# Kernel optimization log

Hardware: AMD Instinct MI355X
Metric: run time of the kernel (lower is better)

Reference implementation:

```python
import jax, jax.numpy as jnp
import numpy as np

B, L, C = 2, 2048, 1024
H = 16
D = C // H  # 64
ROPE_THETA = 10000.0


def _rope_tables(seq_len, head_dim, dtype=jnp.float32):
    # freqs_cis equivalent: angle[t, j] = t * theta^(-2j/head_dim)
    inv_freq = 1.0 / (ROPE_THETA ** (jnp.arange(0, head_dim, 2, dtype=jnp.float32) / head_dim))
    ang = jnp.arange(seq_len, dtype=jnp.float32)[:, None] * inv_freq[None, :]  # [L, D/2]
    return jnp.cos(ang).astype(dtype), jnp.sin(ang).astype(dtype)


def setup_inputs() -> dict:
    key = jax.random.key(0)
    k1, k2, k3 = jax.random.split(key, 3)
    x = jax.random.normal(k1, (B, L, C), dtype=jnp.float32)
    qkv_w = jax.random.normal(k2, (3 * C, C), dtype=jnp.float32) * 0.02
    proj_w = jax.random.normal(k3, (C, C), dtype=jnp.float32) * 0.02
    proj_b = jnp.zeros((C,), dtype=jnp.float32)
    cos, sin = _rope_tables(L, D)
    return {"x": x, "qkv_w": qkv_w, "proj_w": proj_w, "proj_b": proj_b, "cos": cos, "sin": sin}


def _apply_rope(t, cos, sin):
    # t: [B, L, H, D]; cos/sin: [L, D/2]; interleaved complex rotation
    te = t[..., 0::2]
    to = t[..., 1::2]
    c = cos[None, :, None, :]
    s = sin[None, :, None, :]
    re = te * c - to * s
    im = te * s + to * c
    out = jnp.stack([re, im], axis=-1)  # [B, L, H, D/2, 2]
    return out.reshape(t.shape)


def reference(x, qkv_w, proj_w, proj_b, cos, sin):
    b, l, c = x.shape
    scale = (c // H) ** -0.5
    qkv = (x @ qkv_w.T).reshape(b, l, 3, H, c // H)  # [B, L, 3, H, D]
    q, k, v = qkv[:, :, 0], qkv[:, :, 1], qkv[:, :, 2]  # each [B, L, H, D]
    q = _apply_rope(q, cos, sin)
    k = _apply_rope(k, cos, sin)
    # memory_efficient_attention math: softmax(q k^T * scale) v, per head
    logits = jnp.einsum("blhd,bmhd->bhlm", q, k) * scale  # [B, H, L, L]
    p = jax.nn.softmax(logits, axis=-1)
    out = jnp.einsum("bhlm,bmhd->blhd", p, v).reshape(b, l, c)
    return out @ proj_w.T + proj_b
```

## Files before the change

kernel.cpp:

```cpp
#include <hip/hip_runtime.h>


typedef __attribute__((ext_vector_type(8))) short s8v;
typedef __attribute__((ext_vector_type(4))) float f4v;
typedef __attribute__((ext_vector_type(4))) unsigned short u16x4;

__device__ __forceinline__ unsigned short f2bf(float f) {
  unsigned int u = __float_as_uint(f);
  u += 0x7FFFu + ((u >> 16) & 1u);
  return (unsigned short)(u >> 16);
}

__device__ __forceinline__ void gl16(const unsigned short* g, unsigned short* l) {
  __builtin_amdgcn_global_load_lds((const __attribute__((address_space(1))) void*)g,
                                   (__attribute__((address_space(3))) void*)l,
                                   16, 0, 0);
}

__device__ __forceinline__ s8v pack8(const float* p) {
  const float4 a = *reinterpret_cast<const float4*>(p);
  const float4 b = *reinterpret_cast<const float4*>(p + 4);
  s8v r;
  r[0]=(short)f2bf(a.x); r[1]=(short)f2bf(a.y); r[2]=(short)f2bf(a.z); r[3]=(short)f2bf(a.w);
  r[4]=(short)f2bf(b.x); r[5]=(short)f2bf(b.y); r[6]=(short)f2bf(b.z); r[7]=(short)f2bf(b.w);
  return r;
}

#define DPP_F(x, ctrl) \
  __int_as_float(__builtin_amdgcn_update_dpp(0, __float_as_int(x), (ctrl), 0xf, 0xf, false))

__device__ __forceinline__ float row16_max(float x) {
  x = fmaxf(x, DPP_F(x, 0xB1));
  x = fmaxf(x, DPP_F(x, 0x4E));
  x = fmaxf(x, DPP_F(x, 0x124));
  x = fmaxf(x, DPP_F(x, 0x128));
  return x;
}
__device__ __forceinline__ float row16_sum(float x) {
  x += DPP_F(x, 0xB1);
  x += DPP_F(x, 0x4E);
  x += DPP_F(x, 0x124);
  x += DPP_F(x, 0x128);
  return x;
}

__global__ __launch_bounds__(256)
void k_convert(const float* __restrict__ X, const float* __restrict__ W,
               const float* __restrict__ Wp,
               unsigned short* __restrict__ Xb, unsigned short* __restrict__ Wb,
               unsigned short* __restrict__ Wpb)
{
  const int bid = blockIdx.x, tid = threadIdx.x;
  if (bid < 2048) {
    const size_t e = (size_t)bid * 2048 + (size_t)tid * 8;
    *reinterpret_cast<s8v*>(Xb + e) = pack8(X + e);
  } else if (bid < 3584) {
    const size_t e = (size_t)(bid - 2048) * 2048 + (size_t)tid * 8;
    const int p = (int)(e >> 10);
    const int col = (int)(e & 1023);
    int n;
    if (p < 2048) {
      const int t = p >> 10;
      const int hh = (p & 1023) >> 6;
      const int c = p & 63;
      const int d = (c < 32) ? (c << 1) : (((c - 32) << 1) | 1);
      n = (t << 10) + (hh << 6) + d;
    } else {
      n = p;
    }
    *reinterpret_cast<s8v*>(Wb + e) = pack8(W + (size_t)n * 1024 + col);
  } else {
    const size_t e = (size_t)(bid - 3584) * 2048 + (size_t)tid * 8;
    *reinterpret_cast<s8v*>(Wpb + e) = pack8(Wp + e);
  }
}

__global__ __launch_bounds__(256)
void k_gemm_qkv(const unsigned short* __restrict__ Ab,
                const unsigned short* __restrict__ Bb,
                const float* __restrict__ Ct, const float* __restrict__ St,
                unsigned short* __restrict__ qb, unsigned short* __restrict__ kb,
                unsigned short* __restrict__ vt)
{
  __shared__ __align__(16) unsigned short Asm[128 * 32];
  __shared__ __align__(16) unsigned short Bsm[128 * 32];

  const int tid  = threadIdx.x;
  const int w    = tid >> 6;
  const int lane = tid & 63;
  const int lr   = lane & 15;
  const int lg   = lane >> 4;
  const int wm   = w >> 1, wn = w & 1;

  const int row0 = blockIdx.x << 7;
  const int col0 = blockIdx.y << 7;

  const int srow = (w << 5) + (lane >> 2);
  const int scol = (lane & 3) << 3;
  const unsigned short* Ag = Ab + (size_t)(row0 + srow) * 1024 + scol;
  const unsigned short* Bg = Bb + (size_t)(col0 + srow) * 1024 + scol;
  unsigned short* Al0 = &Asm[(w << 5) * 32];
  unsigned short* Al1 = Al0 + 512;
  unsigned short* Bl0 = &Bsm[(w << 5) * 32];
  unsigned short* Bl1 = Bl0 + 512;

  f4v acc[4][4];
#pragma unroll
  for (int m = 0; m < 4; ++m)
#pragma unroll
    for (int n = 0; n < 4; ++n) acc[m][n] = (f4v){0.f, 0.f, 0.f, 0.f};

  for (int k0 = 0; k0 < 1024; k0 += 32) {
    gl16(Ag + k0, Al0);
    gl16(Ag + k0 + 16 * 1024, Al1);
    gl16(Bg + k0, Bl0);
    gl16(Bg + k0 + 16 * 1024, Bl1);
    __syncthreads();

    s8v af[4], bfr[4];
#pragma unroll
    for (int m = 0; m < 4; ++m)
      af[m] = *reinterpret_cast<const s8v*>(&Asm[(wm * 64 + m * 16 + lr) * 32 + lg * 8]);
#pragma unroll
    for (int n = 0; n < 4; ++n)
      bfr[n] = *reinterpret_cast<const s8v*>(&Bsm[(wn * 64 + n * 16 + lr) * 32 + lg * 8]);
#pragma unroll
    for (int m = 0; m < 4; ++m)
#pragma unroll
      for (int n = 0; n < 4; ++n)
        acc[m][n] = __builtin_amdgcn_mfma_f32_16x16x32_bf16(af[m], bfr[n], acc[m][n], 0, 0, 0);
    __syncthreads();
  }

  const int colbase = col0 + wn * 64;
  const int t  = colbase >> 10;
  const int h  = (colbase & 1023) >> 6;

  if (t == 2) {
#pragma unroll
    for (int m = 0; m < 4; ++m) {
      const int token = row0 + wm * 64 + m * 16 + lg * 4;
      const int bI = token >> 11;
      const int lI = token & 2047;
      unsigned short* vbase = vt + (((size_t)bI * 16 + h) * 64) * 2048 + lI;
#pragma unroll
      for (int n = 0; n < 4; ++n) {
        const int d = n * 16 + lr;
        u16x4 pk;
        pk[0] = f2bf(acc[m][n][0]); pk[1] = f2bf(acc[m][n][1]);
        pk[2] = f2bf(acc[m][n][2]); pk[3] = f2bf(acc[m][n][3]);
        *reinterpret_cast<u16x4*>(vbase + (size_t)d * 2048) = pk;
      }
    }
  } else {
    unsigned short* dst = (t == 0) ? qb : kb;
    const float sc = (t == 0) ? 0.18033688011112042f : 1.0f;
#pragma unroll
    for (int m = 0; m < 4; ++m) {
#pragma unroll
      for (int j = 0; j < 4; ++j) {
        const int token = row0 + wm * 64 + m * 16 + lg * 4 + j;
        const int bI = token >> 11;
        const int lI = token & 2047;
        unsigned short* rowp = dst + (((size_t)bI * 16 + h) * 2048 + lI) * 64;
#pragma unroll
        for (int pn = 0; pn < 2; ++pn) {
          const int d2 = pn * 16 + lr;
          const float c = Ct[lI * 32 + d2];
          const float s = St[lI * 32 + d2];
          const float e = acc[m][pn][j];
          const float o = acc[m][pn + 2][j];
          rowp[d2]      = f2bf((e * c - o * s) * sc);
          rowp[32 + d2] = f2bf((e * s + o * c) * sc);
        }
      }
    }
  }
}

__global__ __launch_bounds__(256)
void k_attn(const unsigned short* __restrict__ qb,
            const unsigned short* __restrict__ kb,
            const unsigned short* __restrict__ vt,
            unsigned short* __restrict__ ab)
{
  __shared__ unsigned short Ps[4][16][132];
  __shared__ unsigned short Vt[64][132];

  const int tid  = threadIdx.x;
  const int w    = tid >> 6;
  const int lane = tid & 63;
  const int lr   = lane & 15;
  const int lg   = lane >> 4;

  const int bx = blockIdx.x;
  const int qt = bx & 31;
  const int h  = (bx >> 5) & 15;
  const int b  = bx >> 9;

  const size_t bh = ((size_t)b * 16 + h) * 2048;
  const unsigned short* Qp  = qb + (bh + (size_t)qt * 64 + w * 16) * 64;
  const unsigned short* Kp  = kb + bh * 64;
  const unsigned short* Vg  = vt + bh * 64;

  const s8v qa0 = *reinterpret_cast<const s8v*>(Qp + lr * 64 + 0 + lg * 8);
  const s8v qa1 = *reinterpret_cast<const s8v*>(Qp + lr * 64 + 32 + lg * 8);

  f4v o[4];
#pragma unroll
  for (int i = 0; i < 4; ++i) o[i] = (f4v){0.f, 0.f, 0.f, 0.f};
  float mrow[4] = {-1e30f, -1e30f, -1e30f, -1e30f};
  float lrow[4] = {0.f, 0.f, 0.f, 0.f};

  const int sd = tid >> 2;
  const int sk = (tid & 3) << 3;

  for (int kt = 0; kt < 16; ++kt) {
    const unsigned short* Kt = Kp + (size_t)kt * 128 * 64;

    const unsigned short* vsrc = Vg + (size_t)sd * 2048 + kt * 128 + sk;
    s8v vv[4];
#pragma unroll
    for (int j = 0; j < 4; ++j)
      vv[j] = *reinterpret_cast<const s8v*>(vsrc + j * 32);

    __syncthreads();
#pragma unroll
    for (int j = 0; j < 4; ++j)
      *reinterpret_cast<s8v*>(&Vt[sd][sk + j * 32]) = vv[j];

    f4v s[8];
#pragma unroll
    for (int ct = 0; ct < 8; ++ct) {
      const s8v kf0 = *reinterpret_cast<const s8v*>(Kt + (ct * 16 + lr) * 64 + 0 + lg * 8);
      const s8v kf1 = *reinterpret_cast<const s8v*>(Kt + (ct * 16 + lr) * 64 + 32 + lg * 8);
      f4v z = (f4v){0.f, 0.f, 0.f, 0.f};
      z = __builtin_amdgcn_mfma_f32_16x16x32_bf16(qa0, kf0, z, 0, 0, 0);
      z = __builtin_amdgcn_mfma_f32_16x16x32_bf16(qa1, kf1, z, 0, 0, 0);
      s[ct] = z;
    }

#pragma unroll
    for (int r = 0; r < 4; ++r) {
      float mx = fmaxf(fmaxf(fmaxf(s[0][r], s[1][r]), fmaxf(s[2][r], s[3][r])),
                       fmaxf(fmaxf(s[4][r], s[5][r]), fmaxf(s[6][r], s[7][r])));
      mx = row16_max(mx);
      const float mnew = fmaxf(mrow[r], mx);
      const float corr = exp2f(mrow[r] - mnew);
      mrow[r] = mnew;
      const int rr = lg * 4 + r;
      float rs = 0.f;
#pragma unroll
      for (int ct = 0; ct < 8; ++ct) {
        const float p = exp2f(s[ct][r] - mnew);
        rs += p;
        Ps[w][rr][ct * 16 + lr] = f2bf(p);
      }
      rs = row16_sum(rs);
      lrow[r] = lrow[r] * corr + rs;
      o[0][r] *= corr; o[1][r] *= corr; o[2][r] *= corr; o[3][r] *= corr;
    }
    __syncthreads();

    s8v pa[4];
#pragma unroll
    for (int kc = 0; kc < 4; ++kc)
      pa[kc] = *reinterpret_cast<const s8v*>(&Ps[w][lr][kc * 32 + lg * 8]);
#pragma unroll
    for (int dt = 0; dt < 4; ++dt) {
#pragma unroll
      for (int kc = 0; kc < 4; ++kc) {
        const s8v vbF = *reinterpret_cast<const s8v*>(&Vt[dt * 16 + lr][kc * 32 + lg * 8]);
        o[dt] = __builtin_amdgcn_mfma_f32_16x16x32_bf16(pa[kc], vbF, o[dt], 0, 0, 0);
      }
    }
  }

  const int lbase = qt * 64 + w * 16 + lg * 4;
  unsigned short* obase = ab + (size_t)b * 2048 * 1024 + (size_t)h * 64;
#pragma unroll
  for (int r = 0; r < 4; ++r) {
    const float inv = 1.0f / lrow[r];
    unsigned short* orow = obase + (size_t)(lbase + r) * 1024;
    orow[0 + lr]  = f2bf(o[0][r] * inv);
    orow[16 + lr] = f2bf(o[1][r] * inv);
    orow[32 + lr] = f2bf(o[2][r] * inv);
    orow[48 + lr] = f2bf(o[3][r] * inv);
  }
}

__global__ __launch_bounds__(256)
void k_gemm_proj(const unsigned short* __restrict__ Ab,
                 const unsigned short* __restrict__ Bb,
                 const float* __restrict__ PB, float* __restrict__ OUT)
{
  __shared__ __align__(16) unsigned short Asm[128 * 32];
  __shared__ __align__(16) unsigned short Bsm[128 * 32];

  const int tid  = threadIdx.x;
  const int w    = tid >> 6;
  const int lane = tid & 63;
  const int lr   = lane & 15;
  const int lg   = lane >> 4;
  const int wm   = w >> 1, wn = w & 1;

  const int row0 = blockIdx.x << 7;
  const int col0 = blockIdx.y << 7;

  const int srow = (w << 5) + (lane >> 2);
  const int scol = (lane & 3) << 3;
  const unsigned short* Ag = Ab + (size_t)(row0 + srow) * 1024 + scol;
  const unsigned short* Bg = Bb + (size_t)(col0 + srow) * 1024 + scol;
  unsigned short* Al0 = &Asm[(w << 5) * 32];
  unsigned short* Al1 = Al0 + 512;
  unsigned short* Bl0 = &Bsm[(w << 5) * 32];
  unsigned short* Bl1 = Bl0 + 512;

  f4v acc[4][4];
#pragma unroll
  for (int m = 0; m < 4; ++m)
#pragma unroll
    for (int n = 0; n < 4; ++n) acc[m][n] = (f4v){0.f, 0.f, 0.f, 0.f};

  for (int k0 = 0; k0 < 1024; k0 += 32) {
    gl16(Ag + k0, Al0);
    gl16(Ag + k0 + 16 * 1024, Al1);
    gl16(Bg + k0, Bl0);
    gl16(Bg + k0 + 16 * 1024, Bl1);
    __syncthreads();

    s8v af[4], bfr[4];
#pragma unroll
    for (int m = 0; m < 4; ++m)
      af[m] = *reinterpret_cast<const s8v*>(&Asm[(wm * 64 + m * 16 + lr) * 32 + lg * 8]);
#pragma unroll
    for (int n = 0; n < 4; ++n)
      bfr[n] = *reinterpret_cast<const s8v*>(&Bsm[(wn * 64 + n * 16 + lr) * 32 + lg * 8]);
#pragma unroll
    for (int m = 0; m < 4; ++m)
#pragma unroll
      for (int n = 0; n < 4; ++n)
        acc[m][n] = __builtin_amdgcn_mfma_f32_16x16x32_bf16(af[m], bfr[n], acc[m][n], 0, 0, 0);
    __syncthreads();
  }

  float bias[4];
#pragma unroll
  for (int n = 0; n < 4; ++n) bias[n] = PB[col0 + wn * 64 + n * 16 + lr];

#pragma unroll
  for (int m = 0; m < 4; ++m) {
#pragma unroll
    for (int j = 0; j < 4; ++j) {
      const size_t token = row0 + wm * 64 + m * 16 + lg * 4 + j;
      float* orow = OUT + token * 1024 + col0 + wn * 64 + lr;
#pragma unroll
      for (int n = 0; n < 4; ++n) orow[n * 16] = acc[m][n][j] + bias[n];
    }
  }
}

extern "C" void kernel_launch(void* const* d_in, const int* in_sizes, int n_in,
                              void* d_out, int out_size, void* d_ws, size_t ws_size,
                              hipStream_t stream) {
  const float* X    = (const float*)d_in[0];
  const float* Wqkv = (const float*)d_in[1];
  const float* Wp   = (const float*)d_in[2];
  const float* Pb   = (const float*)d_in[3];
  const float* Ct   = (const float*)d_in[4];
  const float* St   = (const float*)d_in[5];
  float* OUT = (float*)d_out;

  unsigned short* Xb  = (unsigned short*)d_ws;
  unsigned short* Wb  = Xb + (size_t)4194304;
  unsigned short* Wpb = Wb + (size_t)3145728;
  unsigned short* qb  = Wpb + (size_t)1048576;
  unsigned short* kb  = qb + (size_t)4194304;
  unsigned short* vt  = kb + (size_t)4194304;
  unsigned short* ab  = vt + (size_t)4194304;

  k_convert<<<dim3(4096), 256, 0, stream>>>(X, Wqkv, Wp, Xb, Wb, Wpb);
  k_gemm_qkv<<<dim3(32, 24), 256, 0, stream>>>(Xb, Wb, Ct, St, qb, kb, vt);
  k_attn<<<dim3(1024), 256, 0, stream>>>(qb, kb, vt, ab);
  k_gemm_proj<<<dim3(32, 8), 256, 0, stream>>>(ab, Wpb, Pb, OUT);
}
```

Baseline: 286.1 us.

## Double-buffer K/V tile loads in registers and ping-pong V LDS buffers

The attention kernel now prefetches the next K fragments and V slice into registers before computing the current tile, and alternates between two V LDS buffers so the leading __syncthreads can be dropped. The mid-iteration barrier is replaced with an explicit lgkmcnt wait plus s_barrier and a sched_barrier. This is meant to hide global load latency behind MFMA and softmax work. It raises register and LDS use, which may lower occupancy, and the race safety of the V buffer reuse rests on the single barrier per iteration.

```diff
diff --git a/kernel.cpp b/kernel.cpp
--- a/kernel.cpp
+++ b/kernel.cpp
@@ -185,7 +185,8 @@
             unsigned short* __restrict__ ab)
 {
   __shared__ unsigned short Ps[4][16][132];
-  __shared__ unsigned short Vt[64][132];
+  __shared__ unsigned short Vt0[64][132];
+  __shared__ unsigned short Vt1[64][132];
 
   const int tid  = threadIdx.x;
   const int w    = tid >> 6;
@@ -215,28 +216,32 @@
   const int sd = tid >> 2;
   const int sk = (tid & 3) << 3;
 
-  for (int kt = 0; kt < 16; ++kt) {
-    const unsigned short* Kt = Kp + (size_t)kt * 128 * 64;
-
-    const unsigned short* vsrc = Vg + (size_t)sd * 2048 + kt * 128 + sk;
-    s8v vv[4];
+  s8v kfA[8][2], kfB[8][2], vvA[4], vvB[4];
+
+  auto LOAD = [&](s8v (&kf)[8][2], s8v (&vv)[4], int t) {
+    const unsigned short* Kt = Kp + (size_t)t * 128 * 64;
+    const unsigned short* vs = Vg + (size_t)sd * 2048 + t * 128 + sk;
 #pragma unroll
     for (int j = 0; j < 4; ++j)
-      vv[j] = *reinterpret_cast<const s8v*>(vsrc + j * 32);
-
-    __syncthreads();
+      vv[j] = *reinterpret_cast<const s8v*>(vs + j * 32);
+#pragma unroll
+    for (int ct = 0; ct < 8; ++ct) {
+      kf[ct][0] = *reinterpret_cast<const s8v*>(Kt + (ct * 16 + lr) * 64 + 0 + lg * 8);
+      kf[ct][1] = *reinterpret_cast<const s8v*>(Kt + (ct * 16 + lr) * 64 + 32 + lg * 8);
+    }
+  };
+
+  auto ITER = [&](s8v (&kf)[8][2], s8v (&vv)[4], unsigned short (*VT)[132]) {
 #pragma unroll
     for (int j = 0; j < 4; ++j)
-      *reinterpret_cast<s8v*>(&Vt[sd][sk + j * 32]) = vv[j];
+      *reinterpret_cast<s8v*>(&VT[sd][sk + j * 32]) = vv[j];
 
     f4v s[8];
 #pragma unroll
     for (int ct = 0; ct < 8; ++ct) {
-      const s8v kf0 = *reinterpret_cast<const s8v*>(Kt + (ct * 16 + lr) * 64 + 0 + lg * 8);
-      const s8v kf1 = *reinterpret_cast<const s8v*>(Kt + (ct * 16 + lr) * 64 + 32 + lg * 8);
       f4v z = (f4v){0.f, 0.f, 0.f, 0.f};
-      z = __builtin_amdgcn_mfma_f32_16x16x32_bf16(qa0, kf0, z, 0, 0, 0);
-      z = __builtin_amdgcn_mfma_f32_16x16x32_bf16(qa1, kf1, z, 0, 0, 0);
+      z = __builtin_amdgcn_mfma_f32_16x16x32_bf16(qa0, kf[ct][0], z, 0, 0, 0);
+      z = __builtin_amdgcn_mfma_f32_16x16x32_bf16(qa1, kf[ct][1], z, 0, 0, 0);
       s[ct] = z;
     }
 
@@ -260,7 +265,10 @@
       lrow[r] = lrow[r] * corr + rs;
       o[0][r] *= corr; o[1][r] *= corr; o[2][r] *= corr; o[3][r] *= corr;
     }
-    __syncthreads();
+
+    asm volatile("s_waitcnt lgkmcnt(0)" ::: "memory");
+    __builtin_amdgcn_s_barrier();
+    __builtin_amdgcn_sched_barrier(0);
 
     s8v pa[4];
 #pragma unroll
@@ -270,10 +278,18 @@
     for (int dt = 0; dt < 4; ++dt) {
 #pragma unroll
       for (int kc = 0; kc < 4; ++kc) {
-        const s8v vbF = *reinterpret_cast<const s8v*>(&Vt[dt * 16 + lr][kc * 32 + lg * 8]);
+        const s8v vbF = *reinterpret_cast<const s8v*>(&VT[dt * 16 + lr][kc * 32 + lg * 8]);
         o[dt] = __builtin_amdgcn_mfma_f32_16x16x32_bf16(pa[kc], vbF, o[dt], 0, 0, 0);
       }
     }
+  };
+
+  LOAD(kfA, vvA, 0);
+  for (int t = 0; t < 16; t += 2) {
+    LOAD(kfB, vvB, t + 1);
+    ITER(kfA, vvA, Vt0);
+    if (t + 2 < 16) LOAD(kfA, vvA, t + 2);
+    ITER(kfB, vvB, Vt1);
   }
 
   const int lbase = qt * 64 + w * 16 + lg * 4;
```

Result: slower. 438.7 us (+53.3%).
